# Kernel tuning notes

Measured on AMD Instinct MI355X. Metric: run time of the kernel, lower is better.

The kernel has to match this reference:

```python
import jax, jax.numpy as jnp
import numpy as np

DIM = 1024
NH = 8
HD = DIM // NH  # 128
E = 8
EPS = 1e-5


def rope_cos_sin(L, hd):
    # matches RotaryPositionEmbedding: emb = cat([freqs, freqs], -1)
    inv_freq = 1.0 / (10000.0 ** (jnp.arange(0, hd, 2, dtype=jnp.float32) / hd))
    freqs = jnp.arange(L, dtype=jnp.float32)[:, None] * inv_freq[None, :]  # (L, hd/2)
    emb = jnp.concatenate([freqs, freqs], axis=-1)  # (L, hd)
    return jnp.cos(emb), jnp.sin(emb)


def rotate_half(x):
    # interleaved rotate, as in the torch apply_rope
    x1 = x[..., 0::2]
    x2 = x[..., 1::2]
    return jnp.stack((-x2, x1), axis=-1).reshape(x.shape)


def rope(t, cos, sin):
    # t: (B,H,L,D); cos/sin: (L,D)
    return t * cos[None, None] + rotate_half(t) * sin[None, None]


def heads(t):
    B, L, C = t.shape
    return t.reshape(B, L, NH, HD).transpose(0, 2, 1, 3)  # (B,H,L,D)


def setup_inputs() -> dict:
    key = jax.random.key(0)
    ks = jax.random.split(key, 32)
    std = 0.02
    d = {}
    d['x'] = jax.random.normal(ks[0], (16, 512, DIM), jnp.float32)
    d['h_a'] = jax.random.normal(ks[1], (16, 256, DIM), jnp.float32)
    d['h_t'] = jax.random.normal(ks[2], (16, 256, DIM), jnp.float32)
    names = ['qa', 'ka', 'va', 'qt', 'kt', 'vt', 'o', 'ffn']
    for i, n in enumerate(names):
        d['W_' + n] = jax.random.normal(ks[3 + 2 * i], (E, DIM, DIM), jnp.float32) * std
        d['b_' + n] = jax.random.normal(ks[4 + 2 * i], (E, DIM), jnp.float32) * std
    d['gamma'] = jnp.ones((E, DIM), jnp.float32)
    d['beta'] = jnp.zeros((E, DIM), jnp.float32)
    d['gating_factor'] = jnp.zeros((E,), jnp.float32)
    d['expert_idx'] = 3
    return d


def reference(x, h_a, h_t,
              W_qa, b_qa, W_ka, b_ka, W_va, b_va,
              W_qt, b_qt, W_kt, b_kt, W_vt, b_vt,
              W_o, b_o, W_ffn, b_ffn,
              gamma, beta, gating_factor, expert_idx):
    e = expert_idx

    def lin(t, W, b):
        return t @ W[e].T + b[e]

    B, T, C = x.shape
    Ka = h_a.shape[1]
    Kt = h_t.shape[1]

    q_a = heads(lin(x, W_qa, b_qa))        # (B,H,T,D)
    q_t = heads(lin(x, W_qt, b_qt))
    k_a = heads(lin(h_a, W_ka, b_ka))      # (B,H,Ka,D)
    v_a = heads(lin(h_a, W_va, b_va))
    k_t = heads(lin(h_t, W_kt, b_kt))      # (B,H,Kt,D)
    v_t = heads(lin(h_t, W_vt, b_vt))

    cos_m, sin_m = rope_cos_sin(T, HD)
    q_a = rope(q_a, cos_m, sin_m)
    q_t = rope(q_t, cos_m, sin_m)
    cos_a, sin_a = rope_cos_sin(Ka, HD)
    k_a = rope(k_a, cos_a, sin_a)
    cos_t, sin_t = rope_cos_sin(Kt, HD)
    k_t = rope(k_t, cos_t, sin_t)

    ratio_g = jax.nn.sigmoid(gating_factor[e])
    s_a = jnp.einsum('bhtd,bhkd->bhtk', q_a, k_a)
    s_t = jnp.einsum('bhtd,bhkd->bhtk', q_t, k_t) * ratio_g
    scores = jnp.concatenate([s_a, s_t], axis=-1) / np.sqrt(HD)
    w = jax.nn.softmax(scores, axis=-1)            # (B,H,T,Ka+Kt)
    v = jnp.concatenate([v_a, v_t], axis=2)        # (B,H,Ka+Kt,D)
    out = jnp.einsum('bhtk,bhkd->bhtd', w, v)
    out = out.transpose(0, 2, 1, 3).reshape(B, T, C)
    out = lin(out, W_o, b_o)

    x = out + x
    # ffn: SmileMoENorm -> SmileMoELinear -> ReLU (no extra residual)
    mu = jnp.mean(x, axis=-1, keepdims=True)
    var = jnp.var(x, axis=-1, keepdims=True)
    xn = (x - mu) / jnp.sqrt(var + EPS) * gamma[e] + beta[e]
    x = jax.nn.relu(lin(xn, W_ffn, b_ffn))
    return x
```

## Files before the change

### kernel.cpp

```cpp
#include <hip/hip_runtime.h>
#include <stdint.h>

typedef __bf16 bf16x8 __attribute__((ext_vector_type(8)));
typedef float f32x4 __attribute__((ext_vector_type(4)));
typedef unsigned short u16x8 __attribute__((ext_vector_type(8)));

typedef const __attribute__((address_space(1))) void* gas_ptr;
typedef __attribute__((address_space(3))) void* las_ptr;
typedef const __attribute__((address_space(3))) char* lds_c3;

__device__ __forceinline__ void gload16(const void* g, void* l) {
  __builtin_amdgcn_global_load_lds((gas_ptr)g, (las_ptr)l, 16, 0, 0);
}

__device__ __forceinline__ bf16x8 dsread16(const char* p) {
  bf16x8 r;
  asm volatile("ds_read_b128 %0, %1" : "=v"(r) : "v"((lds_c3)p));
  return r;
}
__device__ __forceinline__ void dswrite2(char* p, uint32_t v) {
  asm volatile("ds_write_b16 %0, %1" : : "v"((las_ptr)p), "v"(v));
}
template <int OFF>
__device__ __forceinline__ float dswz(float x) {
  float r;
  asm volatile("ds_swizzle_b32 %0, %1 offset:%c2" : "=v"(r) : "v"(x), "i"(OFF));
  return r;
}

__device__ __forceinline__ unsigned short f2bf(float f) {
  uint32_t u = __float_as_uint(f);
  u += 0x7FFFu + ((u >> 16) & 1u);
  return (unsigned short)(u >> 16);
}

__device__ __forceinline__ void conv8(const float* __restrict__ src,
                                      unsigned short* __restrict__ dst, int i) {
  const float4* s4 = (const float4*)src;
  float4 a = s4[2 * i], b = s4[2 * i + 1];
  u16x8 r;
  r[0] = f2bf(a.x); r[1] = f2bf(a.y); r[2] = f2bf(a.z); r[3] = f2bf(a.w);
  r[4] = f2bf(b.x); r[5] = f2bf(b.y); r[6] = f2bf(b.z); r[7] = f2bf(b.w);
  *(u16x8*)&dst[(size_t)i * 8] = r;
}

__global__ __launch_bounds__(256)
void prep_all(const float* __restrict__ x, const float* __restrict__ h_a,
              const float* __restrict__ h_t,
              const float* W0, const float* W1, const float* W2, const float* W3,
              const float* W4, const float* W5, const float* W6, const float* W7,
              const int* __restrict__ eptr,
              unsigned short* __restrict__ XB, unsigned short* __restrict__ HAB,
              unsigned short* __restrict__ HTB, unsigned short* __restrict__ WW,
              float* __restrict__ cosb, float* __restrict__ sinb) {
  const int blk = blockIdx.x, tid = threadIdx.x;
  if (blk < 4096) {
    conv8(x, XB, blk * 256 + tid);
  } else if (blk < 6144) {
    conv8(h_a, HAB, (blk - 4096) * 256 + tid);
  } else if (blk < 8192) {
    conv8(h_t, HTB, (blk - 6144) * 256 + tid);
  } else if (blk < 12288) {
    const int w = (blk - 8192) >> 9;
    const int i = ((blk - 8192) & 511) * 256 + tid;
    const float* wp;
    switch (w) {
      case 0: wp = W0; break; case 1: wp = W1; break;
      case 2: wp = W2; break; case 3: wp = W3; break;
      case 4: wp = W4; break; case 5: wp = W5; break;
      case 6: wp = W6; break; default: wp = W7; break;
    }
    conv8(wp + (size_t)(*eptr) * 1048576, WW + (size_t)w * 1048576, i);
  } else {
    const int i = (blk - 12288) * 256 + tid;
    const int t = i >> 7, d = i & 127;
    const int f = d & 63;
    float invf = expf(-0.14391156831212787f * (float)f);
    float ang = (float)t * invf;
    float s, c;
    sincosf(ang, &s, &c);
    cosb[i] = c;
    sinb[i] = s;
  }
}

template <int MODE>
__global__ __launch_bounds__(512, 1)
void gemm8p(const unsigned short* __restrict__ A0, const unsigned short* __restrict__ A1,
            const unsigned short* __restrict__ W0, const unsigned short* __restrict__ W1,
            const unsigned short* __restrict__ W2, const unsigned short* __restrict__ W3,
            const float* __restrict__ bias0, const float* __restrict__ bias1,
            const float* __restrict__ bias2, const float* __restrict__ bias3,
            const int* __restrict__ eptr, const float* __restrict__ ctab,
            const float* __restrict__ stab,
            unsigned short* __restrict__ out0, unsigned short* __restrict__ out1,
            unsigned short* __restrict__ outV) {
  __shared__ __align__(16) char AL[65536];
  __shared__ __align__(16) char BL[65536];
  const int tid = threadIdx.x;
  const int lane = tid & 63, wid = tid >> 6, fr = lane & 15, g = lane >> 4;
  const int wm = wid >> 2, wn = wid & 3;
  const int id = blockIdx.x;
  constexpr int CPX = (MODE == 0) ? 32 : 16;
  const int swz = (id & 7) * CPX + (id >> 3);
  const int bm = swz >> 3, bn = swz & 7;
  const int z = (MODE == 1) ? blockIdx.y : 0;
  const int e = *eptr;

  const unsigned short* Asel;
  const unsigned short* Wsel;
  const float* bias;
  const int half = bn >> 2;
  const int cb0 = (bn & 3) * 256;
  if constexpr (MODE == 0) {
    Asel = A0;
    Wsel = half ? W1 : W0;
    bias = (half ? bias1 : bias0) + e * 1024;
  } else {
    Asel = z ? A1 : A0;
    Wsel = z ? (half ? W3 : W2) : (half ? W1 : W0);
    bias = (z ? (half ? bias3 : bias2) : (half ? bias1 : bias0)) + e * 1024;
  }

  const char* Ab = (const char*)Asel + (size_t)bm * 256 * 2048;
  const char* Bb = (const char*)Wsel + (size_t)cb0 * 2048;

  const int sxor = ((tid >> 2) ^ (tid >> 4)) & 3;
  const int csrc = ((tid & 3) ^ sxor) << 4;
  const char* AgsB = Ab + (tid >> 2) * 2048 + csrc;
  const char* BgsB = Bb + (tid >> 2) * 2048 + csrc;
  char* Ald = AL + tid * 16;
  char* Bld = BL + tid * 16;

#define STA(T)                                                   \
  { const char* s_ = AgsB + (T) * 64;                            \
    char* d_ = Ald + ((T) & 3) * 16384;                          \
    gload16(s_, d_); gload16(s_ + 262144, d_ + 8192); }
#define STB(T)                                                   \
  { const char* s_ = BgsB + (T) * 64;                            \
    char* d_ = Bld + ((T) & 3) * 16384;                          \
    gload16(s_, d_); gload16(s_ + 262144, d_ + 8192); }

  const int cread = ((g ^ (fr & 3) ^ ((fr >> 2) & 3)) << 4);
  const int aread = (wm * 128 + fr) * 64 + cread;
  const int bread = (wn * 64 + fr) * 64 + cread;

  f32x4 acc[8][4];
#pragma unroll
  for (int m = 0; m < 8; ++m)
#pragma unroll
    for (int n = 0; n < 4; ++n) acc[m][n] = f32x4{0.f, 0.f, 0.f, 0.f};
  bf16x8 af[8], bfr[4];

#define RDA(BUF)                                                 \
  { const char* p_ = AL + (BUF) * 16384 + aread;                 \
    _Pragma("unroll") for (int m = 0; m < 8; ++m)                \
        af[m] = dsread16(p_ + m * 1024); }
#define RDB(BUF, NH)                                             \
  { const char* p_ = BL + (BUF) * 16384 + bread + (NH) * 2048;   \
    bfr[(NH) * 2]     = dsread16(p_);                            \
    bfr[(NH) * 2 + 1] = dsread16(p_ + 1024); }

  STA(0); STB(0); STA(1); STB(1); STA(2); STB(2);

#pragma unroll 1
  for (int t = 0; t < 32; ++t) {
    __builtin_amdgcn_sched_barrier(0);
    if (t <= 29)      asm volatile("s_waitcnt vmcnt(8)");
    else if (t == 30) asm volatile("s_waitcnt vmcnt(4)");
    else              asm volatile("s_waitcnt vmcnt(0)");
    __builtin_amdgcn_s_barrier();
    __builtin_amdgcn_sched_barrier(0);
    const int buf = t & 3;
    RDA(buf);
    RDB(buf, 0);
    __builtin_amdgcn_sched_barrier(0);
    if (t < 29) STA(t + 3);
    __builtin_amdgcn_sched_barrier(0);
    asm volatile("s_waitcnt lgkmcnt(0)");
    __builtin_amdgcn_sched_barrier(0);
    __builtin_amdgcn_s_setprio(1);
#pragma unroll
    for (int m = 0; m < 8; ++m) {
      acc[m][0] = __builtin_amdgcn_mfma_f32_16x16x32_bf16(af[m], bfr[0], acc[m][0], 0, 0, 0);
      acc[m][1] = __builtin_amdgcn_mfma_f32_16x16x32_bf16(af[m], bfr[1], acc[m][1], 0, 0, 0);
    }
    __builtin_amdgcn_s_setprio(0);
    __builtin_amdgcn_sched_barrier(0);
    RDB(buf, 1);
    __builtin_amdgcn_sched_barrier(0);
    if (t < 29) STB(t + 3);
    __builtin_amdgcn_sched_barrier(0);
    asm volatile("s_waitcnt lgkmcnt(0)");
    __builtin_amdgcn_sched_barrier(0);
    __builtin_amdgcn_s_setprio(1);
#pragma unroll
    for (int m = 0; m < 8; ++m) {
      acc[m][2] = __builtin_amdgcn_mfma_f32_16x16x32_bf16(af[m], bfr[2], acc[m][2], 0, 0, 0);
      acc[m][3] = __builtin_amdgcn_mfma_f32_16x16x32_bf16(af[m], bfr[3], acc[m][3], 0, 0, 0);
    }
    __builtin_amdgcn_s_setprio(0);
  }
#undef RDA
#undef RDB
#undef STA
#undef STB

  const int wrow0 = bm * 256 + wm * 128;
#pragma unroll
  for (int m = 0; m < 8; ++m) {
#pragma unroll
    for (int n = 0; n < 4; ++n) {
      const int gc = cb0 + wn * 64 + n * 16 + fr;
      const float bv = bias[gc];
#pragma unroll
      for (int j = 0; j < 4; ++j) {
        const int grow = wrow0 + m * 16 + g * 4 + j;
        float v = acc[m][n][j] + bv;
        if constexpr (MODE == 0) {
          const int t = grow & 511, bb = grow >> 9;
          const int hh = gc >> 7, dd = gc & 127;
          float pv = __shfl_xor(v, 1);
          float cs = ctab[t * 128 + dd], sn = stab[t * 128 + dd];
          float rh = (dd & 1) ? pv : -pv;
          float o = v * cs + rh * sn;
          unsigned short* dst = half ? out1 : out0;
          dst[(((size_t)(bb * 8 + hh) * 512 + t) << 7) + dd] = f2bf(o);
        } else {
          const int t = grow & 255, bb = grow >> 8;
          const int hh = gc >> 7, dd = gc & 127;
          if (half == 0) {
            float pv = __shfl_xor(v, 1);
            float cs = ctab[t * 128 + dd], sn = stab[t * 128 + dd];
            float rh = (dd & 1) ? pv : -pv;
            float o = v * cs + rh * sn;
            unsigned short* dst = z ? out1 : out0;
            dst[(((size_t)(bb * 8 + hh) * 256 + t) << 7) + dd] = f2bf(o);
          } else {
            outV[(((size_t)(bb * 8 + hh) << 7) + dd) * 512 + z * 256 + t] = f2bf(v);
          }
        }
      }
    }
  }
}

template <int MODE>
__global__ __launch_bounds__(512, 1)
void gemm4p(const unsigned short* __restrict__ A, const unsigned short* __restrict__ W,
            const float* __restrict__ biasb, const int* __restrict__ eptr,
            const float* __restrict__ resid, float* __restrict__ outf) {
  __shared__ __align__(16) char AL[65536];
  __shared__ __align__(16) char BL[32768];
  const int tid = threadIdx.x;
  const int lane = tid & 63, wid = tid >> 6, fr = lane & 15, g = lane >> 4;
  const int wm = wid >> 1, wn = wid & 1;
  const int id = blockIdx.x;
  const int swz = (id & 7) * 32 + (id >> 3);
  const int bm = swz >> 3, bn = swz & 7;
  const int e = *eptr;
  const float* bias = biasb + e * 1024;

  const char* Ab = (const char*)A + (size_t)bm * 256 * 2048;
  const char* Bb = (const char*)W + (size_t)bn * 128 * 2048;

  const int sxor = ((tid >> 2) ^ (tid >> 4)) & 3;
  const int csrc = ((tid & 3) ^ sxor) << 4;
  const char* AgsB = Ab + (tid >> 2) * 2048 + csrc;
  const char* BgsB = Bb + (tid >> 2) * 2048 + csrc;
  char* Ald = AL + tid * 16;
  char* Bld = BL + tid * 16;

#define STA4(T)                                                  \
  { const char* s_ = AgsB + (T) * 64;                            \
    char* d_ = Ald + ((T) & 3) * 16384;                          \
    gload16(s_, d_); gload16(s_ + 262144, d_ + 8192); }
#define STB4(T)                                                  \
  { const char* s_ = BgsB + (T) * 64;                            \
    char* d_ = Bld + ((T) & 3) * 8192;                           \
    gload16(s_, d_); }

  const int cread = ((g ^ (fr & 3) ^ ((fr >> 2) & 3)) << 4);
  const int aread = (wm * 64 + fr) * 64 + cread;
  const int bread = (wn * 64 + fr) * 64 + cread;

  f32x4 acc[4][4];
#pragma unroll
  for (int m = 0; m < 4; ++m)
#pragma unroll
    for (int n = 0; n < 4; ++n) acc[m][n] = f32x4{0.f, 0.f, 0.f, 0.f};
  bf16x8 af[4], bfr[4];

#define RDA4(BUF)                                                \
  { const char* p_ = AL + (BUF) * 16384 + aread;                 \
    _Pragma("unroll") for (int m = 0; m < 4; ++m)                \
        af[m] = dsread16(p_ + m * 1024); }
#define RDB4(BUF)                                                \
  { const char* p_ = BL + (BUF) * 8192 + bread;                  \
    _Pragma("unroll") for (int n = 0; n < 4; ++n)                \
        bfr[n] = dsread16(p_ + n * 1024); }

  STA4(0); STB4(0); STA4(1); STB4(1); STA4(2); STB4(2);

#pragma unroll 1
  for (int t = 0; t < 32; ++t) {
    __builtin_amdgcn_sched_barrier(0);
    if (t <= 29)      asm volatile("s_waitcnt vmcnt(6)");
    else if (t == 30) asm volatile("s_waitcnt vmcnt(3)");
    else              asm volatile("s_waitcnt vmcnt(0)");
    __builtin_amdgcn_s_barrier();
    __builtin_amdgcn_sched_barrier(0);
    const int buf = t & 3;
    RDA4(buf);
    RDB4(buf);
    __builtin_amdgcn_sched_barrier(0);
    if (t < 29) { STA4(t + 3); STB4(t + 3); }
    __builtin_amdgcn_sched_barrier(0);
    asm volatile("s_waitcnt lgkmcnt(0)");
    __builtin_amdgcn_sched_barrier(0);
    __builtin_amdgcn_s_setprio(1);
#pragma unroll
    for (int m = 0; m < 4; ++m)
#pragma unroll
      for (int n = 0; n < 4; ++n)
        acc[m][n] = __builtin_amdgcn_mfma_f32_16x16x32_bf16(af[m], bfr[n], acc[m][n], 0, 0, 0);
    __builtin_amdgcn_s_setprio(0);
  }
#undef RDA4
#undef RDB4
#undef STA4
#undef STB4

  const int wrow0 = bm * 256 + wm * 64;
#pragma unroll
  for (int m = 0; m < 4; ++m) {
#pragma unroll
    for (int n = 0; n < 4; ++n) {
      const int gc = bn * 128 + wn * 64 + n * 16 + fr;
      const float bv = bias[gc];
#pragma unroll
      for (int j = 0; j < 4; ++j) {
        const int grow = wrow0 + m * 16 + g * 4 + j;
        float v = acc[m][n][j] + bv;
        const size_t idx = ((size_t)grow << 10) + gc;
        if constexpr (MODE == 2) outf[idx] = v + resid[idx];
        else outf[idx] = fmaxf(v, 0.f);
      }
    }
  }
}

__global__ __launch_bounds__(256, 2)
void attn_kernel(const unsigned short* __restrict__ QA, const unsigned short* __restrict__ QT,
                 const unsigned short* __restrict__ KA, const unsigned short* __restrict__ KT,
                 const unsigned short* __restrict__ VT,
                 unsigned short* __restrict__ AO,
                 const float* __restrict__ gating, const int* __restrict__ eptr) {
  __shared__ unsigned short Ks[2][8192];
  __shared__ unsigned short Vs[2][8192];
  __shared__ unsigned short Ps[8192];
  const int tid = threadIdx.x, lane = tid & 63, wv = tid >> 6;
  const int fr = lane & 15, g = lane >> 4;
  const int bid = blockIdx.x;
  const int b = bid >> 5, h = (bid >> 2) & 7, q0 = (bid & 3) << 7;
  const float ratio = 1.f / (1.f + __expf(-gating[*eptr]));
  const float SC = 0.08838834764831845f;
  const size_t bh = (size_t)(b * 8 + h);

  bf16x8 qf[2][4];
  {
    const char* qa = (const char*)QA + ((bh * 512 + q0 + wv * 32 + fr) << 8) + g * 16;
#pragma unroll
    for (int mb = 0; mb < 2; ++mb)
#pragma unroll
      for (int kb = 0; kb < 4; ++kb)
        qf[mb][kb] = *(const bf16x8*)(qa + mb * 4096 + kb * 64);
  }

  auto stage = [&](int t, int buf) {
    const char* kgb = (const char*)((t < 4) ? KA : KT) + ((bh * 256 + ((size_t)(t & 3) << 6)) << 8);
    const char* vgb = (const char*)VT + (bh << 17) + (t << 7);
    char* ksd = (char*)Ks[buf] + tid * 16;
    char* vsd = (char*)Vs[buf] + tid * 16;
#pragma unroll
    for (int j = 0; j < 4; ++j) {
      const int rk = j * 16 + (tid >> 4);
      const int ck = ((tid & 15) << 4) ^ ((rk & 7) << 4);
      gload16(kgb + rk * 256 + ck, ksd + j * 4096);
      const int dv = j * 32 + (tid >> 3);
      const int cv = ((tid & 7) << 4) ^ ((dv & 7) << 4);
      gload16(vgb + dv * 1024 + cv, vsd + j * 4096);
    }
  };

  float m_run[2][4], l_run[2][4];
  f32x4 oacc[2][8];
#pragma unroll
  for (int mb = 0; mb < 2; ++mb) {
#pragma unroll
    for (int j = 0; j < 4; ++j) { m_run[mb][j] = -1e30f; l_run[mb][j] = 0.f; }
#pragma unroll
    for (int db = 0; db < 8; ++db) oacc[mb][db] = f32x4{0.f, 0.f, 0.f, 0.f};
  }

  stage(0, 0);

  for (int it = 0; it < 8; ++it) {
    const int cur = it & 1;
    if (it < 7) stage(it + 1, cur ^ 1);
    __builtin_amdgcn_sched_barrier(0);
    if (it < 7) asm volatile("s_waitcnt vmcnt(8)");
    else        asm volatile("s_waitcnt vmcnt(0)");
    __builtin_amdgcn_sched_barrier(0);
    __builtin_amdgcn_s_barrier();
    __builtin_amdgcn_sched_barrier(0);

    if (it == 4) {
      const char* qt = (const char*)QT + ((bh * 512 + q0 + wv * 32 + fr) << 8) + g * 16;
#pragma unroll
      for (int mb = 0; mb < 2; ++mb)
#pragma unroll
        for (int kb = 0; kb < 4; ++kb)
          qf[mb][kb] = *(const bf16x8*)(qt + mb * 4096 + kb * 64);
    }
    const float sc = (it < 4) ? SC : SC * ratio;
    const char* kc = (const char*)Ks[cur];
    const char* vc = (const char*)Vs[cur];

    f32x4 s[2][4];
#pragma unroll
    for (int mb = 0; mb < 2; ++mb)
#pragma unroll
      for (int nb = 0; nb < 4; ++nb) s[mb][nb] = f32x4{0.f, 0.f, 0.f, 0.f};
    bf16x8 kfa[4], kfb[4];
#pragma unroll
    for (int kb = 0; kb < 4; ++kb) {
      const int byt = (fr * 256 + kb * 64 + g * 16) ^ ((fr & 7) << 4);
      kfa[kb] = dsread16(kc + byt);
    }
#pragma unroll
    for (int nb = 0; nb < 4; ++nb) {
      if (nb < 3) {
#pragma unroll
        for (int kb = 0; kb < 4; ++kb) {
          const int r = (nb + 1) * 16 + fr;
          const int byt = (r * 256 + kb * 64 + g * 16) ^ ((r & 7) << 4);
          if (nb & 1) kfa[kb] = dsread16(kc + byt);
          else        kfb[kb] = dsread16(kc + byt);
        }
        asm volatile("s_waitcnt lgkmcnt(4)");
      } else {
        asm volatile("s_waitcnt lgkmcnt(0)");
      }
      __builtin_amdgcn_sched_barrier(0);
      __builtin_amdgcn_s_setprio(1);
#pragma unroll
      for (int kb = 0; kb < 4; ++kb) {
        bf16x8 kf = (nb & 1) ? kfb[kb] : kfa[kb];
        s[0][nb] = __builtin_amdgcn_mfma_f32_16x16x32_bf16(qf[0][kb], kf, s[0][nb], 0, 0, 0);
        s[1][nb] = __builtin_amdgcn_mfma_f32_16x16x32_bf16(qf[1][kb], kf, s[1][nb], 0, 0, 0);
      }
      __builtin_amdgcn_s_setprio(0);
    }
    __builtin_amdgcn_sched_barrier(0);

    float red[8];
#pragma unroll
    for (int mb = 0; mb < 2; ++mb)
#pragma unroll
      for (int j = 0; j < 4; ++j) {
        float mx = -1e30f;
#pragma unroll
        for (int nb = 0; nb < 4; ++nb) {
          s[mb][nb][j] *= sc;
          mx = fmaxf(mx, s[mb][nb][j]);
        }
        red[mb * 4 + j] = mx;
      }
#define MAXR(OFF)                                                        \
    { float tmp[8];                                                      \
      _Pragma("unroll") for (int k = 0; k < 8; ++k) tmp[k] = dswz<OFF>(red[k]); \
      asm volatile("s_waitcnt lgkmcnt(0)");                              \
      __builtin_amdgcn_sched_barrier(0);                                 \
      _Pragma("unroll") for (int k = 0; k < 8; ++k) red[k] = fmaxf(red[k], tmp[k]); }
    MAXR(0x041F) MAXR(0x081F) MAXR(0x101F) MAXR(0x201F)
#undef MAXR
#pragma unroll
    for (int mb = 0; mb < 2; ++mb)
#pragma unroll
      for (int j = 0; j < 4; ++j) {
        const float mn = fmaxf(m_run[mb][j], red[mb * 4 + j]);
        const float alpha = __expf(m_run[mb][j] - mn);
        m_run[mb][j] = mn;
        l_run[mb][j] *= alpha;
#pragma unroll
        for (int db = 0; db < 8; ++db) oacc[mb][db][j] *= alpha;
      }
#pragma unroll
    for (int mb = 0; mb < 2; ++mb)
#pragma unroll
      for (int nb = 0; nb < 4; ++nb)
#pragma unroll
        for (int j = 0; j < 4; ++j) {
          float p = __expf(s[mb][nb][j] - m_run[mb][j]);
          l_run[mb][j] += p;
          const int r = wv * 32 + mb * 16 + g * 4 + j;
          const int byt = (r * 128 + (nb * 16 + fr) * 2) ^ ((r & 7) << 4);
          dswrite2((char*)Ps + byt, (uint32_t)f2bf(p));
        }

#pragma unroll
    for (int kb2 = 0; kb2 < 2; ++kb2) {
      bf16x8 pf[2], vf[8];
#pragma unroll
      for (int mb = 0; mb < 2; ++mb) {
        const int r = wv * 32 + mb * 16 + fr;
        const int byt = (r * 128 + kb2 * 64 + g * 16) ^ ((r & 7) << 4);
        pf[mb] = dsread16((const char*)Ps + byt);
      }
#pragma unroll
      for (int db = 0; db < 8; ++db) {
        const int rv = db * 16 + fr;
        const int byt = (rv * 128 + kb2 * 64 + g * 16) ^ ((rv & 7) << 4);
        vf[db] = dsread16(vc + byt);
      }
      asm volatile("s_waitcnt lgkmcnt(0)");
      __builtin_amdgcn_sched_barrier(0);
      __builtin_amdgcn_s_setprio(1);
#pragma unroll
      for (int db = 0; db < 8; ++db) {
        oacc[0][db] = __builtin_amdgcn_mfma_f32_16x16x32_bf16(pf[0], vf[db], oacc[0][db], 0, 0, 0);
        oacc[1][db] = __builtin_amdgcn_mfma_f32_16x16x32_bf16(pf[1], vf[db], oacc[1][db], 0, 0, 0);
      }
      __builtin_amdgcn_s_setprio(0);
    }
    __builtin_amdgcn_sched_barrier(0);
    __builtin_amdgcn_s_barrier();
  }

#pragma unroll
  for (int mb = 0; mb < 2; ++mb)
#pragma unroll
    for (int j = 0; j < 4; ++j) {
      float lt = l_run[mb][j];
#pragma unroll
      for (int d = 1; d < 16; d <<= 1) lt += __shfl_xor(lt, d);
      float inv = 1.f / lt;
#pragma unroll
      for (int db = 0; db < 8; ++db) {
        float o = oacc[mb][db][j] * inv;
        int row = q0 + wv * 32 + mb * 16 + g * 4 + j;
        int col = h * 128 + db * 16 + fr;
        AO[(((size_t)b * 512 + row) << 10) + col] = f2bf(o);
      }
    }
}

__global__ __launch_bounds__(256)
void ln_kernel(const float* __restrict__ X2, const float* __restrict__ gbase,
               const float* __restrict__ bbase, const int* __restrict__ eptr,
               unsigned short* __restrict__ XN) {
  const int row = blockIdx.x, tid = threadIdx.x;
  const float* x = X2 + ((size_t)row << 10);
  float4 v = ((const float4*)x)[tid];
  float s = v.x + v.y + v.z + v.w;
  float ss = v.x * v.x + v.y * v.y + v.z * v.z + v.w * v.w;
#pragma unroll
  for (int d = 1; d < 64; d <<= 1) {
    s += __shfl_xor(s, d);
    ss += __shfl_xor(ss, d);
  }
  __shared__ float red[8];
  const int wv = tid >> 6, lane = tid & 63;
  if (lane == 0) { red[wv] = s; red[4 + wv] = ss; }
  __syncthreads();
  s = red[0] + red[1] + red[2] + red[3];
  ss = red[4] + red[5] + red[6] + red[7];
  const float mu = s * 0.0009765625f;
  const float var = ss * 0.0009765625f - mu * mu;
  const float inv = rsqrtf(var + 1e-5f);
  const int e = *eptr;
  const float* gg = gbase + e * 1024 + tid * 4;
  const float* bb = bbase + e * 1024 + tid * 4;
  ushort4 o;
  o.x = f2bf((v.x - mu) * inv * gg[0] + bb[0]);
  o.y = f2bf((v.y - mu) * inv * gg[1] + bb[1]);
  o.z = f2bf((v.z - mu) * inv * gg[2] + bb[2]);
  o.w = f2bf((v.w - mu) * inv * gg[3] + bb[3]);
  *(ushort4*)&XN[((size_t)row << 10) + tid * 4] = o;
}

extern "C" void kernel_launch(void* const* d_in, const int* in_sizes, int n_in,
                              void* d_out, int out_size, void* d_ws, size_t ws_size,
                              hipStream_t stream) {
  (void)in_sizes; (void)n_in; (void)out_size; (void)ws_size;
  const float* x      = (const float*)d_in[0];
  const float* h_a    = (const float*)d_in[1];
  const float* h_t    = (const float*)d_in[2];
  const float* W_qa   = (const float*)d_in[3];
  const float* b_qa   = (const float*)d_in[4];
  const float* W_ka   = (const float*)d_in[5];
  const float* b_ka   = (const float*)d_in[6];
  const float* W_va   = (const float*)d_in[7];
  const float* b_va   = (const float*)d_in[8];
  const float* W_qt   = (const float*)d_in[9];
  const float* b_qt   = (const float*)d_in[10];
  const float* W_kt   = (const float*)d_in[11];
  const float* b_kt   = (const float*)d_in[12];
  const float* W_vt   = (const float*)d_in[13];
  const float* b_vt   = (const float*)d_in[14];
  const float* W_o    = (const float*)d_in[15];
  const float* b_o    = (const float*)d_in[16];
  const float* W_ffn  = (const float*)d_in[17];
  const float* b_ffn  = (const float*)d_in[18];
  const float* gamma  = (const float*)d_in[19];
  const float* beta   = (const float*)d_in[20];
  const float* gating = (const float*)d_in[21];
  const int*   eptr   = (const int*)d_in[22];

  char* ws = (char*)d_ws;
  unsigned short* XB  = (unsigned short*)(ws + 0);
  unsigned short* HAB = (unsigned short*)(ws + 16777216);
  unsigned short* HTB = (unsigned short*)(ws + 25165824);
  float*          X2  = (float*)(ws + 0);
  unsigned short* WW  = (unsigned short*)(ws + 33554432);
  unsigned short* QAb = (unsigned short*)(ws + 50331648);
  unsigned short* XN  = QAb;
  unsigned short* QTb = (unsigned short*)(ws + 67108864);
  unsigned short* KAb = (unsigned short*)(ws + 83886080);
  unsigned short* KTb = (unsigned short*)(ws + 92274688);
  unsigned short* VTb = (unsigned short*)(ws + 100663296);
  unsigned short* AOb = (unsigned short*)(ws + 117440512);
  float* COS = (float*)(ws + 134217728);
  float* SIN = (float*)(ws + 134479872);

  prep_all<<<12544, 256, 0, stream>>>(x, h_a, h_t,
      W_qa, W_ka, W_va, W_qt, W_kt, W_vt, W_o, W_ffn, eptr,
      XB, HAB, HTB, WW, COS, SIN);

  gemm8p<0><<<dim3(256), 512, 0, stream>>>(XB, nullptr,
      WW + 0ull * 1048576, WW + 3ull * 1048576, nullptr, nullptr,
      b_qa, b_qt, nullptr, nullptr, eptr, COS, SIN,
      QAb, QTb, nullptr);

  gemm8p<1><<<dim3(128, 2), 512, 0, stream>>>(HAB, HTB,
      WW + 1ull * 1048576, WW + 2ull * 1048576,
      WW + 4ull * 1048576, WW + 5ull * 1048576,
      b_ka, b_va, b_kt, b_vt, eptr, COS, SIN,
      KAb, KTb, VTb);

  attn_kernel<<<512, 256, 0, stream>>>(QAb, QTb, KAb, KTb, VTb, AOb, gating, eptr);

  gemm4p<2><<<dim3(256), 512, 0, stream>>>(AOb, WW + 6ull * 1048576, b_o, eptr, x, X2);

  ln_kernel<<<8192, 256, 0, stream>>>(X2, gamma, beta, eptr, XN);

  gemm4p<3><<<dim3(256), 512, 0, stream>>>(XN, WW + 7ull * 1048576, b_ffn, eptr,
                                           nullptr, (float*)d_out);
}
```

Before: 232.8 us.

## Switch GEMM mainloops to K=64 double-buffered tiles with ping-pong barriers

Both GEMM kernels move from a 4-stage ring of K=32 LDS tiles to 2-stage buffers of K=64 tiles, with a new 8-way XOR swizzle for 128-byte rows. Each K-step is split into four MFMA phases separated by workgroup barriers, in an HipKittens-style ping-pong schedule that interleaves global-to-LDS loads with compute. The aim is fewer loop iterations and barrier/waitcnt overheads per FLOP and better LDS bank behaviour. In exchange, prefetch depth drops to a single tile, and the added barriers and the full vmcnt(0) wait at the end of each iteration may expose memory latency.

Result: no change. 237.0 us (+1.8%).

```diff
diff --git a/kernel.cpp b/kernel.cpp
--- a/kernel.cpp
+++ b/kernel.cpp
@@ -125,84 +125,87 @@
   const char* Ab = (const char*)Asel + (size_t)bm * 256 * 2048;
   const char* Bb = (const char*)Wsel + (size_t)cb0 * 2048;
 
-  const int sxor = ((tid >> 2) ^ (tid >> 4)) & 3;
-  const int csrc = ((tid & 3) ^ sxor) << 4;
-  const char* AgsB = Ab + (tid >> 2) * 2048 + csrc;
-  const char* BgsB = Bb + (tid >> 2) * 2048 + csrc;
+  const int csw = (((tid & 7) ^ (((tid >> 3) & 1) << 2) ^ (((tid >> 5) & 1) << 1)) << 4);
+  const char* Ags = Ab + (tid >> 3) * 2048 + csw;
+  const char* Bgs = Bb + (tid >> 3) * 2048 + csw;
   char* Ald = AL + tid * 16;
   char* Bld = BL + tid * 16;
 
-#define STA(T)                                                   \
-  { const char* s_ = AgsB + (T) * 64;                            \
-    char* d_ = Ald + ((T) & 3) * 16384;                          \
-    gload16(s_, d_); gload16(s_ + 262144, d_ + 8192); }
-#define STB(T)                                                   \
-  { const char* s_ = BgsB + (T) * 64;                            \
-    char* d_ = Bld + ((T) & 3) * 16384;                          \
-    gload16(s_, d_); gload16(s_ + 262144, d_ + 8192); }
-
-  const int cread = ((g ^ (fr & 3) ^ ((fr >> 2) & 3)) << 4);
-  const int aread = (wm * 128 + fr) * 64 + cread;
-  const int bread = (wn * 64 + fr) * 64 + cread;
+#define STA(T)                                                              \
+  { const char* s_ = Ags + (T) * 128;                                       \
+    char* d_ = Ald + ((T) & 1) * 32768;                                     \
+    gload16(s_, d_);           gload16(s_ + 131072, d_ + 8192);             \
+    gload16(s_ + 262144, d_ + 16384); gload16(s_ + 393216, d_ + 24576); }
+#define STB(T)                                                              \
+  { const char* s_ = Bgs + (T) * 128;                                       \
+    char* d_ = Bld + ((T) & 1) * 32768;                                     \
+    gload16(s_, d_);           gload16(s_ + 131072, d_ + 8192);             \
+    gload16(s_ + 262144, d_ + 16384); gload16(s_ + 393216, d_ + 24576); }
+
+  const int lsw = ((fr & 1) << 2) ^ (((fr >> 2) & 1) << 1);
+  const int cs0 = ((0 * 4 + g) ^ lsw) << 4;
+  const int cs1 = ((1 * 4 + g) ^ lsw) << 4;
+  const int arow = (wm * 128 + fr) * 128;
+  const int brow = (wn * 64 + fr) * 128;
 
   f32x4 acc[8][4];
 #pragma unroll
   for (int m = 0; m < 8; ++m)
 #pragma unroll
     for (int n = 0; n < 4; ++n) acc[m][n] = f32x4{0.f, 0.f, 0.f, 0.f};
-  bf16x8 af[8], bfr[4];
-
-#define RDA(BUF)                                                 \
-  { const char* p_ = AL + (BUF) * 16384 + aread;                 \
-    _Pragma("unroll") for (int m = 0; m < 8; ++m)                \
-        af[m] = dsread16(p_ + m * 1024); }
-#define RDB(BUF, NH)                                             \
-  { const char* p_ = BL + (BUF) * 16384 + bread + (NH) * 2048;   \
-    bfr[(NH) * 2]     = dsread16(p_);                            \
-    bfr[(NH) * 2 + 1] = dsread16(p_ + 1024); }
-
-  STA(0); STB(0); STA(1); STB(1); STA(2); STB(2);
+  bf16x8 af[8], bfr[2];
+
+#define RDA(BUF, CS)                                                        \
+  { const char* p_ = AL + (BUF) * 32768 + arow + (CS);                      \
+    _Pragma("unroll") for (int m = 0; m < 8; ++m)                           \
+        af[m] = dsread16(p_ + m * 2048); }
+#define RDB(BUF, CS, NH)                                                    \
+  { const char* p_ = BL + (BUF) * 32768 + brow + (NH) * 4096 + (CS);        \
+    bfr[0] = dsread16(p_);                                                  \
+    bfr[1] = dsread16(p_ + 2048); }
+
+#define MF16(NH)                                                            \
+  __builtin_amdgcn_s_setprio(1);                                            \
+  _Pragma("unroll") for (int m = 0; m < 8; ++m) {                           \
+    acc[m][(NH)*2]   = __builtin_amdgcn_mfma_f32_16x16x32_bf16(             \
+        af[m], bfr[0], acc[m][(NH)*2], 0, 0, 0);                            \
+    acc[m][(NH)*2+1] = __builtin_amdgcn_mfma_f32_16x16x32_bf16(             \
+        af[m], bfr[1], acc[m][(NH)*2+1], 0, 0, 0);                          \
+  }                                                                         \
+  __builtin_amdgcn_s_setprio(0);
+
+#define SB __builtin_amdgcn_sched_barrier(0)
+#define BAR __builtin_amdgcn_s_barrier()
+#define LGK0 asm volatile("s_waitcnt lgkmcnt(0)")
+
+  STA(0); STB(0);
+  SB;
+  asm volatile("s_waitcnt vmcnt(0)");
+  BAR;
 
 #pragma unroll 1
-  for (int t = 0; t < 32; ++t) {
-    __builtin_amdgcn_sched_barrier(0);
-    if (t <= 29)      asm volatile("s_waitcnt vmcnt(8)");
-    else if (t == 30) asm volatile("s_waitcnt vmcnt(4)");
-    else              asm volatile("s_waitcnt vmcnt(0)");
-    __builtin_amdgcn_s_barrier();
-    __builtin_amdgcn_sched_barrier(0);
-    const int buf = t & 3;
-    RDA(buf);
-    RDB(buf, 0);
-    __builtin_amdgcn_sched_barrier(0);
-    if (t < 29) STA(t + 3);
-    __builtin_amdgcn_sched_barrier(0);
-    asm volatile("s_waitcnt lgkmcnt(0)");
-    __builtin_amdgcn_sched_barrier(0);
-    __builtin_amdgcn_s_setprio(1);
-#pragma unroll
-    for (int m = 0; m < 8; ++m) {
-      acc[m][0] = __builtin_amdgcn_mfma_f32_16x16x32_bf16(af[m], bfr[0], acc[m][0], 0, 0, 0);
-      acc[m][1] = __builtin_amdgcn_mfma_f32_16x16x32_bf16(af[m], bfr[1], acc[m][1], 0, 0, 0);
-    }
-    __builtin_amdgcn_s_setprio(0);
-    __builtin_amdgcn_sched_barrier(0);
-    RDB(buf, 1);
-    __builtin_amdgcn_sched_barrier(0);
-    if (t < 29) STB(t + 3);
-    __builtin_amdgcn_sched_barrier(0);
-    asm volatile("s_waitcnt lgkmcnt(0)");
-    __builtin_amdgcn_sched_barrier(0);
-    __builtin_amdgcn_s_setprio(1);
-#pragma unroll
-    for (int m = 0; m < 8; ++m) {
-      acc[m][2] = __builtin_amdgcn_mfma_f32_16x16x32_bf16(af[m], bfr[2], acc[m][2], 0, 0, 0);
-      acc[m][3] = __builtin_amdgcn_mfma_f32_16x16x32_bf16(af[m], bfr[3], acc[m][3], 0, 0, 0);
-    }
-    __builtin_amdgcn_s_setprio(0);
+  for (int t = 0; t < 16; ++t) {
+    const int buf = t & 1;
+    RDA(buf, cs0); RDB(buf, cs0, 0); SB;
+    if (t < 15) STA(t + 1);
+    SB; BAR; LGK0; SB;
+    MF16(0) SB; BAR;
+    RDB(buf, cs0, 1); SB;
+    if (t < 15) STB(t + 1);
+    SB; BAR; LGK0; SB;
+    MF16(1) SB; BAR;
+    RDA(buf, cs1); RDB(buf, cs1, 0); SB;
+    BAR; LGK0; SB;
+    MF16(0) SB; BAR;
+    RDB(buf, cs1, 1); SB;
+    BAR; LGK0; SB;
+    MF16(1) SB;
+    if (t < 15) { asm volatile("s_waitcnt vmcnt(0)"); }
+    BAR;
   }
 #undef RDA
 #undef RDB
+#undef MF16
 #undef STA
 #undef STB
 
@@ -264,72 +267,87 @@
   const char* Ab = (const char*)A + (size_t)bm * 256 * 2048;
   const char* Bb = (const char*)W + (size_t)bn * 128 * 2048;
 
-  const int sxor = ((tid >> 2) ^ (tid >> 4)) & 3;
-  const int csrc = ((tid & 3) ^ sxor) << 4;
-  const char* AgsB = Ab + (tid >> 2) * 2048 + csrc;
-  const char* BgsB = Bb + (tid >> 2) * 2048 + csrc;
+  const int csw = (((tid & 7) ^ (((tid >> 3) & 1) << 2) ^ (((tid >> 5) & 1) << 1)) << 4);
+  const char* Ags = Ab + (tid >> 3) * 2048 + csw;
+  const char* Bgs = Bb + (tid >> 3) * 2048 + csw;
   char* Ald = AL + tid * 16;
   char* Bld = BL + tid * 16;
 
-#define STA4(T)                                                  \
-  { const char* s_ = AgsB + (T) * 64;                            \
-    char* d_ = Ald + ((T) & 3) * 16384;                          \
-    gload16(s_, d_); gload16(s_ + 262144, d_ + 8192); }
-#define STB4(T)                                                  \
-  { const char* s_ = BgsB + (T) * 64;                            \
-    char* d_ = Bld + ((T) & 3) * 8192;                           \
-    gload16(s_, d_); }
-
-  const int cread = ((g ^ (fr & 3) ^ ((fr >> 2) & 3)) << 4);
-  const int aread = (wm * 64 + fr) * 64 + cread;
-  const int bread = (wn * 64 + fr) * 64 + cread;
+#define STA4(T)                                                             \
+  { const char* s_ = Ags + (T) * 128;                                       \
+    char* d_ = Ald + ((T) & 1) * 32768;                                     \
+    gload16(s_, d_);           gload16(s_ + 131072, d_ + 8192);             \
+    gload16(s_ + 262144, d_ + 16384); gload16(s_ + 393216, d_ + 24576); }
+#define STB4(T)                                                             \
+  { const char* s_ = Bgs + (T) * 128;                                       \
+    char* d_ = Bld + ((T) & 1) * 16384;                                     \
+    gload16(s_, d_);           gload16(s_ + 131072, d_ + 8192); }
+
+  const int lsw = ((fr & 1) << 2) ^ (((fr >> 2) & 1) << 1);
+  const int cs0 = ((0 * 4 + g) ^ lsw) << 4;
+  const int cs1 = ((1 * 4 + g) ^ lsw) << 4;
+  const int arow = (wm * 64 + fr) * 128;
+  const int brow = (wn * 64 + fr) * 128;
 
   f32x4 acc[4][4];
 #pragma unroll
   for (int m = 0; m < 4; ++m)
 #pragma unroll
     for (int n = 0; n < 4; ++n) acc[m][n] = f32x4{0.f, 0.f, 0.f, 0.f};
-  bf16x8 af[4], bfr[4];
-
-#define RDA4(BUF)                                                \
-  { const char* p_ = AL + (BUF) * 16384 + aread;                 \
-    _Pragma("unroll") for (int m = 0; m < 4; ++m)                \
-        af[m] = dsread16(p_ + m * 1024); }
-#define RDB4(BUF)                                                \
-  { const char* p_ = BL + (BUF) * 8192 + bread;                  \
-    _Pragma("unroll") for (int n = 0; n < 4; ++n)                \
-        bfr[n] = dsread16(p_ + n * 1024); }
-
-  STA4(0); STB4(0); STA4(1); STB4(1); STA4(2); STB4(2);
+  bf16x8 af[4], bfr[2];
+
+#define RDA4(BUF, CS)                                                       \
+  { const char* p_ = AL + (BUF) * 32768 + arow + (CS);                      \
+    _Pragma("unroll") for (int m = 0; m < 4; ++m)                           \
+        af[m] = dsread16(p_ + m * 2048); }
+#define RDB4(BUF, CS, NH)                                                   \
+  { const char* p_ = BL + (BUF) * 16384 + brow + (NH) * 4096 + (CS);        \
+    bfr[0] = dsread16(p_);                                                  \
+    bfr[1] = dsread16(p_ + 2048); }
+
+#define MF8(NH)                                                             \
+  __builtin_amdgcn_s_setprio(1);                                            \
+  _Pragma("unroll") for (int m = 0; m < 4; ++m) {                           \
+    acc[m][(NH)*2]   = __builtin_amdgcn_mfma_f32_16x16x32_bf16(             \
+        af[m], bfr[0], acc[m][(NH)*2], 0, 0, 0);                            \
+    acc[m][(NH)*2+1] = __builtin_amdgcn_mfma_f32_16x16x32_bf16(             \
+        af[m], bfr[1], acc[m][(NH)*2+1], 0, 0, 0);                          \
+  }                                                                         \
+  __builtin_amdgcn_s_setprio(0);
+
+  STA4(0); STB4(0);
+  __builtin_amdgcn_sched_barrier(0);
+  asm volatile("s_waitcnt vmcnt(0)");
+  __builtin_amdgcn_s_barrier();
 
 #pragma unroll 1
-  for (int t = 0; t < 32; ++t) {
-    __builtin_amdgcn_sched_barrier(0);
-    if (t <= 29)      asm volatile("s_waitcnt vmcnt(6)");
-    else if (t == 30) asm volatile("s_waitcnt vmcnt(3)");
-    else              asm volatile("s_waitcnt vmcnt(0)");
-    __builtin_amdgcn_s_barrier();
-    __builtin_amdgcn_sched_barrier(0);
-    const int buf = t & 3;
-    RDA4(buf);
-    RDB4(buf);
-    __builtin_amdgcn_sched_barrier(0);
-    if (t < 29) { STA4(t + 3); STB4(t + 3); }
-    __builtin_amdgcn_sched_barrier(0);
-    asm volatile("s_waitcnt lgkmcnt(0)");
-    __builtin_amdgcn_sched_barrier(0);
-    __builtin_amdgcn_s_setprio(1);
-#pragma unroll
-    for (int m = 0; m < 4; ++m)
-#pragma unroll
-      for (int n = 0; n < 4; ++n)
-        acc[m][n] = __builtin_amdgcn_mfma_f32_16x16x32_bf16(af[m], bfr[n], acc[m][n], 0, 0, 0);
-    __builtin_amdgcn_s_setprio(0);
+  for (int t = 0; t < 16; ++t) {
+    const int buf = t & 1;
+    RDA4(buf, cs0); RDB4(buf, cs0, 0); SB;
+    if (t < 15) STA4(t + 1);
+    SB; BAR; LGK0; SB;
+    MF8(0) SB; BAR;
+    RDB4(buf, cs0, 1); SB;
+    if (t < 15) STB4(t + 1);
+    SB; BAR; LGK0; SB;
+    MF8(1) SB; BAR;
+    RDA4(buf, cs1); RDB4(buf, cs1, 0); SB;
+    BAR; LGK0; SB;
+    MF8(0) SB; BAR;
+    RDB4(buf, cs1, 1); SB;
+    BAR; LGK0; SB;
+    MF8(1) SB;
+    if (t < 15) { asm volatile("s_waitcnt vmcnt(0)"); }
+    BAR;
   }
 #undef RDA4
 #undef RDB4
+#undef MF8
 #undef STA4
 #undef STB4
+#undef SB
+#undef BAR
+#undef LGK0
 
   const int wrow0 = bm * 256 + wm * 64;
 #pragma unroll
```
